# Performance work log

Measured on AMD Instinct MI355X. Metric: run time of the kernel, lower is better.

The kernel has to match this reference:

```python
import jax, jax.numpy as jnp
import numpy as np

USER_NUM = 100000
ITEM_NUM = 50000
N_EDGES = 2000000
EMB = 64
N_LAYERS = 3


def setup_inputs() -> dict:
    key = jax.random.key(0)
    k1, k2, k3, k4 = jax.random.split(key, 4)
    # xavier-uniform-like init scale for embeddings
    scale = float(np.sqrt(6.0 / (USER_NUM + EMB)))
    user_emb = jax.random.uniform(k1, (USER_NUM, EMB), jnp.float32, -scale, scale)
    scale_i = float(np.sqrt(6.0 / (ITEM_NUM + EMB)))
    item_emb = jax.random.uniform(k2, (ITEM_NUM, EMB), jnp.float32, -scale_i, scale_i)
    u_idx = jax.random.randint(k3, (N_EDGES,), 0, USER_NUM, jnp.int32)
    i_idx = jax.random.randint(k4, (N_EDGES,), 0, ITEM_NUM, jnp.int32)
    return {"user_emb": user_emb, "item_emb": item_emb, "u_idx": u_idx, "i_idx": i_idx}


def _degree_norms(u_idx, i_idx):
    ones = jnp.ones(u_idx.shape[0], jnp.float32)
    d_u = jax.ops.segment_sum(ones, u_idx, num_segments=USER_NUM)
    d_i = jax.ops.segment_sum(ones, i_idx, num_segments=ITEM_NUM)
    d_u = jnp.where(d_u == 0, 1.0, d_u)
    d_i = jnp.where(d_i == 0, 1.0, d_i)
    return ((1.0 / d_u)[:, None], (1.0 / d_i)[:, None],
            (d_u ** -0.5)[:, None], (d_i ** -0.5)[:, None])


def reference(user_emb, item_emb, u_idx, i_idx):
    d_u_inv, d_i_inv, d_u_inv_sqrt, d_i_inv_sqrt = _degree_norms(u_idx, i_idx)

    # SpMM via gather + segment_sum on the edge list (binary interaction values)
    def spmm_rt(x_u):  # (rt @ x_u): [U,D] -> [I,D]
        return jax.ops.segment_sum(x_u[u_idx], i_idx, num_segments=ITEM_NUM)

    def spmm_r(x_i):  # (r @ x_i): [I,D] -> [U,D]
        return jax.ops.segment_sum(x_i[i_idx], u_idx, num_segments=USER_NUM)

    user_e = user_emb
    item_e = item_emb
    sum_u = user_e
    sum_i = item_e
    for _ in range(N_LAYERS):
        # user propagation: u -> hyperedge(items) -> u
        tmp_u = user_e * d_u_inv_sqrt
        tmp_i = spmm_rt(tmp_u) * d_i_inv
        user_e = spmm_r(tmp_i) * d_u_inv_sqrt
        sum_u = sum_u + user_e
        # item propagation: i -> hyperedge(users) -> i
        tmp_i2 = item_e * d_i_inv_sqrt
        tmp_u2 = spmm_r(tmp_i2) * d_u_inv
        item_e = spmm_rt(tmp_u2) * d_i_inv_sqrt
        sum_i = sum_i + item_e
    inv = 1.0 / (N_LAYERS + 1)
    return sum_u * inv, sum_i * inv
```

## Files before the change

kernel.cpp:

```cpp
#include <hip/hip_runtime.h>
#include <hip/hip_fp16.h>
#include <math.h>

#define U_NUM 100000
#define I_NUM 50000
#define NE    2000000
#define EMB   64
#define NLAYERS 3

#define BSH   7
#define BROWS 128
#define NBU_U ((U_NUM + BROWS - 1) >> BSH)
#define NBU_I ((I_NUM + BROWS - 1) >> BSH)
#define NBU_T (NBU_U + NBU_I)
#define PACK_SH 17
#define PACK_MASK 0x1FFFF

#define CAP_U 4096
#define CAP_I 6144

#define CHUNK2 2048
#define NBLK2 ((NE + CHUNK2 - 1) / CHUNK2)

#define DBINS 512

#define ND_U ((U_NUM + 2047) / 2048)
#define ND_I ((I_NUM + 2047) / 2048)
#define NINIT (((U_NUM + I_NUM) * (EMB / 4) + 255) / 256)

#define FP8_SCALE 512.0f

typedef float v2f __attribute__((ext_vector_type(2)));

static inline int ceil_div(int a, int b){ return (a + b - 1) / b; }


__global__ void binfill_k(const int* __restrict__ u_idx, const int* __restrict__ i_idx,
                          int* __restrict__ bcur_u, int* __restrict__ bcur_i,
                          int* __restrict__ bin_u, int* __restrict__ bin_i){
  __shared__ int scnt[NBU_T];
  __shared__ int gbase[NBU_T];
  __shared__ int scur[NBU_T];
  int t = threadIdx.x;
  for (int k = t; k < NBU_T; k += 256){ scnt[k] = 0; scur[k] = 0; }
  __syncthreads();
  int e0 = blockIdx.x * CHUNK2 + t * 8;
  int u[8], iv[8];
  bool act = e0 < NE;
  if (act){
    int4 a = *(const int4*)(u_idx + e0);
    int4 b = *(const int4*)(u_idx + e0 + 4);
    int4 c = *(const int4*)(i_idx + e0);
    int4 d = *(const int4*)(i_idx + e0 + 4);
    u[0]=a.x; u[1]=a.y; u[2]=a.z; u[3]=a.w; u[4]=b.x; u[5]=b.y; u[6]=b.z; u[7]=b.w;
    iv[0]=c.x; iv[1]=c.y; iv[2]=c.z; iv[3]=c.w; iv[4]=d.x; iv[5]=d.y; iv[6]=d.z; iv[7]=d.w;
#pragma unroll
    for (int k = 0; k < 8; ++k){
      atomicAdd(&scnt[u[k] >> BSH], 1);
      atomicAdd(&scnt[NBU_U + (iv[k] >> BSH)], 1);
    }
  }
  __syncthreads();
  for (int k = t; k < NBU_T; k += 256){
    int c = scnt[k];
    if (c){
      int* bc = (k < NBU_U) ? (bcur_u + k) : (bcur_i + (k - NBU_U));
      gbase[k] = atomicAdd(bc, c);
    }
  }
  __syncthreads();
  if (act){
#pragma unroll
    for (int k = 0; k < 8; ++k){
      int bu = u[k] >> BSH;
      int p = atomicAdd(&scur[bu], 1);
      bin_u[(size_t)bu * CAP_U + gbase[bu] + p] =
          ((u[k] & (BROWS - 1)) << PACK_SH) | iv[k];
      int bi = NBU_U + (iv[k] >> BSH);
      int p2 = atomicAdd(&scur[bi], 1);
      bin_i[(size_t)(bi - NBU_U) * CAP_I + gbase[bi] + p2] =
          ((iv[k] & (BROWS - 1)) << PACK_SH) | u[k];
    }
  }
}

__global__ void small_scan2_k(const int* __restrict__ cA, int* __restrict__ oA,
                              int* __restrict__ rA, int nA,
                              const int* __restrict__ cB, int* __restrict__ oB,
                              int* __restrict__ rB, int nB){
  const int* cnt; int* offs; int* cur; int n;
  if (blockIdx.x == 0){ cnt = cA; offs = oA; cur = rA; n = nA; }
  else { cnt = cB; offs = oB; cur = rB; n = nB; }
  __shared__ int s[1024];
  int t = threadIdx.x;
  int v = (t < n) ? cnt[t] : 0;
  s[t] = v; __syncthreads();
  for (int o = 1; o < 1024; o <<= 1){
    int x = (t >= o) ? s[t - o] : 0;
    __syncthreads();
    s[t] += x;
    __syncthreads();
  }
  int excl = (t > 0) ? s[t - 1] : 0;
  if (t < n){ offs[t] = excl; cur[t] = excl; }
  if (t == n - 1) offs[n] = s[t];
}


__global__ void bucket_build_k(const int* __restrict__ bin_u, const int* __restrict__ bin_i,
                               const int* __restrict__ bcnt_u, const int* __restrict__ bcnt_i,
                               const int* __restrict__ boffs_u, const int* __restrict__ boffs_i,
                               int* __restrict__ cnt_u, int* __restrict__ cnt_i,
                               int* __restrict__ offs_u, int* __restrict__ offs_i,
                               float* __restrict__ du_inv, float* __restrict__ du_invs,
                               float* __restrict__ di_inv, float* __restrict__ di_invs,
                               int* __restrict__ adj_u, int* __restrict__ adj_i,
                               int* __restrict__ dhist_u, int* __restrict__ dhist_i){
  __shared__ int h[BROWS];
  __shared__ int part[256];
  __shared__ int dh[DBINS];
  int b = blockIdx.x;
  const int* bin; const int* bcnt; const int* boffs; int* cnt; int* offs;
  float* inv; float* invs; int* adj; int* dhist; int jj, nrows; size_t cap;
  if (b < NBU_U){
    bin = bin_u; bcnt = bcnt_u; boffs = boffs_u; cnt = cnt_u; offs = offs_u;
    inv = du_inv; invs = du_invs; adj = adj_u; dhist = dhist_u; jj = b; nrows = U_NUM; cap = CAP_U;
  } else {
    bin = bin_i; bcnt = bcnt_i; boffs = boffs_i; cnt = cnt_i; offs = offs_i;
    inv = di_inv; invs = di_invs; adj = adj_i; dhist = dhist_i; jj = b - NBU_U; nrows = I_NUM; cap = CAP_I;
  }
  int tid = threadIdx.x;
  int r0 = jj << BSH;
  const int* binb = bin + (size_t)jj * cap;
  int ne = bcnt[jj];
  int badj = boffs[jj];
  if (tid < BROWS) h[tid] = 0;
  for (int t = tid; t < DBINS; t += 256) dh[t] = 0;
  __syncthreads();
  for (int e = tid; e < ne; e += 256)
    atomicAdd(&h[((unsigned)binb[e]) >> PACK_SH], 1);
  __syncthreads();
  int c = (tid < BROWS) ? h[tid] : 0;
  part[tid] = c; __syncthreads();
  for (int o = 1; o < 256; o <<= 1){
    int x = (tid >= o) ? part[tid - o] : 0;
    __syncthreads();
    part[tid] += x;
    __syncthreads();
  }
  int excl = (tid > 0) ? part[tid - 1] : 0;
  if (tid < BROWS){
    h[tid] = excl;
    int row = r0 + tid;
    if (row < nrows){
      cnt[row] = c;
      offs[row] = badj + excl;
      float d = (c > 0) ? (float)c : 1.0f;
      inv[row]  = 1.0f / d;
      invs[row] = 1.0f / sqrtf(d);
      atomicAdd(&dh[min(c, DBINS - 1)], 1);
    } else if (row == nrows){
      offs[row] = badj + excl;
    }
  }
  __syncthreads();
  for (int e = tid; e < ne; e += 256){
    int v = binb[e];
    int slot = badj + atomicAdd(&h[((unsigned)v) >> PACK_SH], 1);
    adj[slot] = v & PACK_MASK;
  }
  __syncthreads();
  for (int t = tid; t < DBINS; t += 256) if (dh[t]) atomicAdd(&dhist[t], dh[t]);
}


__device__ __forceinline__ unsigned pack4_fp8(float a, float b, float c, float d){
  int p = 0;
  p = __builtin_amdgcn_cvt_pk_fp8_f32(a, b, p, false);
  p = __builtin_amdgcn_cvt_pk_fp8_f32(c, d, p, true);
  return (unsigned)p;
}

__device__ __forceinline__ void accq(float* a, uint2 q){
  v2f f0 = __builtin_amdgcn_cvt_pk_f32_fp8(q.x, false);
  v2f f1 = __builtin_amdgcn_cvt_pk_f32_fp8(q.x, true);
  v2f f2 = __builtin_amdgcn_cvt_pk_f32_fp8(q.y, false);
  v2f f3 = __builtin_amdgcn_cvt_pk_f32_fp8(q.y, true);
  a[0] += f0.x; a[1] += f0.y; a[2] += f1.x; a[3] += f1.y;
  a[4] += f2.x; a[5] += f2.y; a[6] += f3.x; a[7] += f3.y;
}


__global__ void post_k(const int* __restrict__ cnt_u, const int* __restrict__ offs_u,
                       const int* __restrict__ dhist_u, int* __restrict__ dcur_u,
                       int4* __restrict__ rd_u,
                       const int* __restrict__ cnt_i, const int* __restrict__ offs_i,
                       const int* __restrict__ dhist_i, int* __restrict__ dcur_i,
                       int4* __restrict__ rd_i,
                       const float* __restrict__ ue, const float* __restrict__ ie,
                       const float* __restrict__ dus, const float* __restrict__ dis,
                       float* __restrict__ out, unsigned char* __restrict__ u0,
                       unsigned char* __restrict__ i0){
  int b = blockIdx.x;
  int t = threadIdx.x;
  if (b >= ND_U + ND_I){
    int idx4 = (b - ND_U - ND_I) * 256 + t;
    const int nu4 = U_NUM * (EMB / 4);
    const int tot4 = (U_NUM + I_NUM) * (EMB / 4);
    if (idx4 >= tot4) return;
    const float* e; unsigned char* hp; float s; int loc;
    if (idx4 < nu4){ e = ue; hp = u0; loc = idx4; s = dus[idx4 >> 4] * FP8_SCALE; }
    else { e = ie; hp = i0; loc = idx4 - nu4; s = dis[(idx4 - nu4) >> 4] * FP8_SCALE; }
    float4 v = ((const float4*)e)[loc];
    ((float4*)out)[idx4] = make_float4(v.x * 0.25f, v.y * 0.25f, v.z * 0.25f, v.w * 0.25f);
    ((unsigned*)hp)[loc] = pack4_fp8(v.x * s, v.y * s, v.z * s, v.w * s);
    return;
  }
  const int* cnt; const int* offs; const int* dhist; int* dcur; int4* rd; int n, base;
  if (b < ND_U){ cnt = cnt_u; offs = offs_u; dhist = dhist_u; dcur = dcur_u; rd = rd_u; n = U_NUM; base = b * 2048; }
  else { cnt = cnt_i; offs = offs_i; dhist = dhist_i; dcur = dcur_i; rd = rd_i; n = I_NUM; base = (b - ND_U) * 2048; }
  __shared__ int sc[DBINS];
  __shared__ int h[DBINS];
  __shared__ int base_s[DBINS];
  sc[t] = dhist[t]; sc[t + 256] = dhist[t + 256];
  h[t] = 0; h[t + 256] = 0;
  __syncthreads();
  for (int o = 1; o < DBINS; o <<= 1){
    int x0 = (t >= o) ? sc[t - o] : 0;
    int x1 = ((t + 256) >= o) ? sc[t + 256 - o] : 0;
    __syncthreads();
    sc[t] += x0; sc[t + 256] += x1;
    __syncthreads();
  }
  int end = min(base + 2048, n);
  for (int r = base + t; r < end; r += 256)
    atomicAdd(&h[min(cnt[r], DBINS - 1)], 1);
  __syncthreads();
  for (int tt = t; tt < DBINS; tt += 256){
    int c = h[tt];
    int excl = tt ? sc[tt - 1] : 0;
    base_s[tt] = c ? (excl + atomicAdd(&dcur[tt], c)) : 0;
    h[tt] = 0;
  }
  __syncthreads();
  for (int r = base + t; r < end; r += 256){
    int c = cnt[r];
    int bb = min(c, DBINS - 1);
    int pos = base_s[bb] + atomicAdd(&h[bb], 1);
    int bg = offs[r];
    rd[n - 1 - pos] = make_int4(bg, bg + c, r, 0);
  }
}


__global__ void spmm_pair(
    const int4* __restrict__ rdA, const int* __restrict__ adjA,
    const unsigned char* __restrict__ srcA, const float* __restrict__ phA,
    unsigned char* __restrict__ dstA, int nA,
    const int4* __restrict__ rdB, const int* __restrict__ adjB,
    const unsigned char* __restrict__ srcB, const float* __restrict__ phB,
    unsigned char* __restrict__ dstB, int nB){
  int t = blockIdx.x * blockDim.x + threadIdx.x;
  int rid = t >> 3;
  int lane = t & 7;
  const int4* rd; const int* adj; const unsigned char* src; const float* ph;
  unsigned char* dst;
  if (rid < nA){
    rd = rdA; adj = adjA; src = srcA; ph = phA; dst = dstA;
  } else {
    rid -= nA;
    if (rid >= nB) return;
    rd = rdB; adj = adjB; src = srcB; ph = phB; dst = dstB;
  }
  int4 d = rd[rid];
  int beg = d.x, end = d.y, row = d.z;
  const unsigned char* sp8 = src + (size_t)(lane << 3);
  float acc[8];
#pragma unroll
  for (int k = 0; k < 8; ++k) acc[k] = 0.f;
  int j = beg;
  for (; j + 7 < end; j += 8){
    int n0 = adj[j],   n1 = adj[j+1], n2 = adj[j+2], n3 = adj[j+3];
    int n4 = adj[j+4], n5 = adj[j+5], n6 = adj[j+6], n7 = adj[j+7];
    uint2 q0 = *(const uint2*)(sp8 + (((size_t)n0) << 6));
    uint2 q1 = *(const uint2*)(sp8 + (((size_t)n1) << 6));
    uint2 q2 = *(const uint2*)(sp8 + (((size_t)n2) << 6));
    uint2 q3 = *(const uint2*)(sp8 + (((size_t)n3) << 6));
    uint2 q4 = *(const uint2*)(sp8 + (((size_t)n4) << 6));
    uint2 q5 = *(const uint2*)(sp8 + (((size_t)n5) << 6));
    uint2 q6 = *(const uint2*)(sp8 + (((size_t)n6) << 6));
    uint2 q7 = *(const uint2*)(sp8 + (((size_t)n7) << 6));
    accq(acc, q0); accq(acc, q1); accq(acc, q2); accq(acc, q3);
    accq(acc, q4); accq(acc, q5); accq(acc, q6); accq(acc, q7);
  }
  for (; j < end; ++j){
    int n0 = adj[j];
    uint2 q0 = *(const uint2*)(sp8 + (((size_t)n0) << 6));
    accq(acc, q0);
  }
  float phv = ph[row];
  unsigned lo = pack4_fp8(acc[0] * phv, acc[1] * phv, acc[2] * phv, acc[3] * phv);
  unsigned hi = pack4_fp8(acc[4] * phv, acc[5] * phv, acc[6] * phv, acc[7] * phv);
  *(uint2*)(dst + (((size_t)row) << 6) + (size_t)(lane << 3)) = make_uint2(lo, hi);
}


__global__ void merge_k(const unsigned char* __restrict__ u1, const unsigned char* __restrict__ u2,
                        const unsigned char* __restrict__ u3,
                        const unsigned char* __restrict__ i1, const unsigned char* __restrict__ i2,
                        const unsigned char* __restrict__ i3,
                        const float* __restrict__ du_inv, const float* __restrict__ du_invs,
                        const float* __restrict__ di_inv, const float* __restrict__ di_invs,
                        float* __restrict__ out){
  int idx4 = blockIdx.x * blockDim.x + threadIdx.x;
  const int nu4 = U_NUM * (EMB / 4);
  const int tot4 = (U_NUM + I_NUM) * (EMB / 4);
  if (idx4 >= tot4) return;
  const unsigned char *t1, *t2, *t3; float ratio; int loc;
  if (idx4 < nu4){
    t1 = u1; t2 = u2; t3 = u3; loc = idx4;
    int row = idx4 >> 4;
    ratio = (0.25f / FP8_SCALE) * du_invs[row] / du_inv[row];
  } else {
    loc = idx4 - nu4;
    t1 = i1; t2 = i2; t3 = i3;
    int row = loc >> 4;
    ratio = (0.25f / FP8_SCALE) * di_invs[row] / di_inv[row];
  }
  unsigned q1 = ((const unsigned*)t1)[loc];
  unsigned q2 = ((const unsigned*)t2)[loc];
  unsigned q3 = ((const unsigned*)t3)[loc];
  float4 o = ((float4*)out)[idx4];
  v2f a, b;
  a = __builtin_amdgcn_cvt_pk_f32_fp8(q1, false); b = __builtin_amdgcn_cvt_pk_f32_fp8(q1, true);
  o.x += ratio * a.x; o.y += ratio * a.y; o.z += ratio * b.x; o.w += ratio * b.y;
  a = __builtin_amdgcn_cvt_pk_f32_fp8(q2, false); b = __builtin_amdgcn_cvt_pk_f32_fp8(q2, true);
  o.x += ratio * a.x; o.y += ratio * a.y; o.z += ratio * b.x; o.w += ratio * b.y;
  a = __builtin_amdgcn_cvt_pk_f32_fp8(q3, false); b = __builtin_amdgcn_cvt_pk_f32_fp8(q3, true);
  o.x += ratio * a.x; o.y += ratio * a.y; o.z += ratio * b.x; o.w += ratio * b.y;
  ((float4*)out)[idx4] = o;
}


extern "C" void kernel_launch(void* const* d_in, const int* in_sizes, int n_in,
                              void* d_out, int out_size, void* d_ws, size_t ws_size,
                              hipStream_t stream){
  const float* user_emb = (const float*)d_in[0];
  const float* item_emb = (const float*)d_in[1];
  const int*   u_idx    = (const int*)d_in[2];
  const int*   i_idx    = (const int*)d_in[3];
  float* out = (float*)d_out;

  char* w = (char*)d_ws;
  size_t off = 0;
  auto alloc = [&](size_t bytes) -> void* {
    void* p = (void*)(w + off);
    off += (bytes + 255) & ~(size_t)255;
    return p;
  };
  int* zb      = (int*)alloc((size_t)(NBU_T + 4 * DBINS) * 4);
  int* bcur_u  = zb;
  int* bcur_i  = bcur_u + NBU_U;
  int* dhist_u = bcur_i + NBU_I;
  int* dhist_i = dhist_u + DBINS;
  int* dcur_u  = dhist_i + DBINS;
  int* dcur_i  = dcur_u + DBINS;
  int* boffs_u = (int*)alloc((size_t)(NBU_U + 1) * 4);
  int* boffs_i = (int*)alloc((size_t)(NBU_I + 1) * 4);
  int* scr_u   = (int*)alloc((size_t)NBU_U * 4);
  int* scr_i   = (int*)alloc((size_t)NBU_I * 4);
  int* cnt_u   = (int*)alloc((size_t)U_NUM * 4);
  int* cnt_i   = (int*)alloc((size_t)I_NUM * 4);
  int* offs_u  = (int*)alloc((size_t)(U_NUM + 1) * 4);
  int* offs_i  = (int*)alloc((size_t)(I_NUM + 1) * 4);
  int4* rd_u   = (int4*)alloc((size_t)U_NUM * 16);
  int4* rd_i   = (int4*)alloc((size_t)I_NUM * 16);
  int* adj_u   = (int*)alloc((size_t)NE * 4);
  int* adj_i   = (int*)alloc((size_t)NE * 4);
  float* du_inv  = (float*)alloc((size_t)U_NUM * 4);
  float* du_invs = (float*)alloc((size_t)U_NUM * 4);
  float* di_inv  = (float*)alloc((size_t)I_NUM * 4);
  float* di_invs = (float*)alloc((size_t)I_NUM * 4);
  const size_t URB = (size_t)U_NUM * EMB;
  const size_t IRB = (size_t)I_NUM * EMB;
  unsigned char* hreg = (unsigned char*)alloc(4 * URB + 4 * IRB + URB + IRB);
  unsigned char* u0 = hreg;
  unsigned char* u1 = u0 + URB;
  unsigned char* u2 = u1 + URB;
  unsigned char* u3 = u2 + URB;
  unsigned char* i0 = u3 + URB;
  unsigned char* i1 = i0 + IRB;
  unsigned char* i2 = i1 + IRB;
  unsigned char* i3 = i2 + IRB;
  unsigned char* tmp_i = i3 + IRB;
  unsigned char* tmp_u = tmp_i + IRB;
  int* bin_u = (int*)hreg;
  int* bin_i = bin_u + (size_t)NBU_U * CAP_U;

  hipMemsetAsync(zb, 0, (size_t)(NBU_T + 4 * DBINS) * 4, stream);
  binfill_k<<<NBLK2, 256, 0, stream>>>(u_idx, i_idx, bcur_u, bcur_i, bin_u, bin_i);
  small_scan2_k<<<2, 1024, 0, stream>>>(bcur_u, boffs_u, scr_u, NBU_U,
                                        bcur_i, boffs_i, scr_i, NBU_I);
  bucket_build_k<<<NBU_T, 256, 0, stream>>>(bin_u, bin_i, bcur_u, bcur_i,
                                            boffs_u, boffs_i,
                                            cnt_u, cnt_i, offs_u, offs_i,
                                            du_inv, du_invs, di_inv, di_invs,
                                            adj_u, adj_i, dhist_u, dhist_i);

  post_k<<<ND_U + ND_I + NINIT, 256, 0, stream>>>(
      cnt_u, offs_u, dhist_u, dcur_u, rd_u,
      cnt_i, offs_i, dhist_i, dcur_i, rd_i,
      user_emb, item_emb, du_invs, di_invs, out, u0, i0);

  const int pair_grid = ceil_div((U_NUM + I_NUM) * 8, 256);
  unsigned char* uls[4] = { u0, u1, u2, u3 };
  unsigned char* ils[4] = { i0, i1, i2, i3 };
  for (int l = 0; l < NLAYERS; ++l){
    spmm_pair<<<pair_grid, 256, 0, stream>>>(
        rd_i, adj_i, uls[l], di_inv, tmp_i, I_NUM,
        rd_u, adj_u, ils[l], du_inv, tmp_u, U_NUM);
    spmm_pair<<<pair_grid, 256, 0, stream>>>(
        rd_u, adj_u, tmp_i, du_inv, uls[l + 1], U_NUM,
        rd_i, adj_i, tmp_u, di_inv, ils[l + 1], I_NUM);
  }

  merge_k<<<NINIT, 256, 0, stream>>>(u1, u2, u3, i1, i2, i3,
                                     du_inv, du_invs, di_inv, di_invs, out);
}
```

Measured before the change: 492.1 us.

## Enlarge binfill and bucket_build blocks; defer layer-0 output to merge

binfill now processes 8192 edges per 1024-thread block, cutting block count and the per-block global atomics on bucket cursors. bucket_build uses 512 threads per block. The layer-0 contribution (emb*0.25) is no longer written to the output in post_k and read back in merge_k; merge_k reads the original fp32 embeddings directly. This removes one full-size output write and read, at the cost of more LDS and scan work per block and possibly lower occupancy.

Measured after the change: 468.8 us, median of 2. 4.7% less time.

```diff
diff --git a/kernel.cpp b/kernel.cpp
--- a/kernel.cpp
+++ b/kernel.cpp
@@ -19,10 +19,11 @@
 #define CAP_U 4096
 #define CAP_I 6144
 
-#define CHUNK2 2048
+#define CHUNK2 8192
 #define NBLK2 ((NE + CHUNK2 - 1) / CHUNK2)
 
 #define DBINS 512
+#define BBT   512
 
 #define ND_U ((U_NUM + 2047) / 2048)
 #define ND_I ((I_NUM + 2047) / 2048)
@@ -42,11 +43,13 @@
   __shared__ int gbase[NBU_T];
   __shared__ int scur[NBU_T];
   int t = threadIdx.x;
-  for (int k = t; k < NBU_T; k += 256){ scnt[k] = 0; scur[k] = 0; }
-  __syncthreads();
-  int e0 = blockIdx.x * CHUNK2 + t * 8;
+  for (int k = t; k < NBU_T; k += 1024){ scnt[k] = 0; scur[k] = 0; }
+  __syncthreads();
+  int base = blockIdx.x * CHUNK2;
+  int end = min(base + CHUNK2, NE);
+  int e0 = base + t * 8;
+  bool act = e0 < end;
   int u[8], iv[8];
-  bool act = e0 < NE;
   if (act){
     int4 a = *(const int4*)(u_idx + e0);
     int4 b = *(const int4*)(u_idx + e0 + 4);
@@ -61,7 +64,7 @@
     }
   }
   __syncthreads();
-  for (int k = t; k < NBU_T; k += 256){
+  for (int k = t; k < NBU_T; k += 1024){
     int c = scnt[k];
     if (c){
       int* bc = (k < NBU_U) ? (bcur_u + k) : (bcur_i + (k - NBU_U));
@@ -117,7 +120,7 @@
                                int* __restrict__ adj_u, int* __restrict__ adj_i,
                                int* __restrict__ dhist_u, int* __restrict__ dhist_i){
   __shared__ int h[BROWS];
-  __shared__ int part[256];
+  __shared__ int part[BBT];
   __shared__ int dh[DBINS];
   int b = blockIdx.x;
   const int* bin; const int* bcnt; const int* boffs; int* cnt; int* offs;
@@ -135,14 +138,14 @@
   int ne = bcnt[jj];
   int badj = boffs[jj];
   if (tid < BROWS) h[tid] = 0;
-  for (int t = tid; t < DBINS; t += 256) dh[t] = 0;
-  __syncthreads();
-  for (int e = tid; e < ne; e += 256)
+  if (tid < DBINS) dh[tid] = 0;
+  __syncthreads();
+  for (int e = tid; e < ne; e += BBT)
     atomicAdd(&h[((unsigned)binb[e]) >> PACK_SH], 1);
   __syncthreads();
   int c = (tid < BROWS) ? h[tid] : 0;
   part[tid] = c; __syncthreads();
-  for (int o = 1; o < 256; o <<= 1){
+  for (int o = 1; o < BBT; o <<= 1){
     int x = (tid >= o) ? part[tid - o] : 0;
     __syncthreads();
     part[tid] += x;
@@ -164,13 +167,13 @@
     }
   }
   __syncthreads();
-  for (int e = tid; e < ne; e += 256){
+  for (int e = tid; e < ne; e += BBT){
     int v = binb[e];
     int slot = badj + atomicAdd(&h[((unsigned)v) >> PACK_SH], 1);
     adj[slot] = v & PACK_MASK;
   }
   __syncthreads();
-  for (int t = tid; t < DBINS; t += 256) if (dh[t]) atomicAdd(&dhist[t], dh[t]);
+  if (tid < DBINS && dh[tid]) atomicAdd(&dhist[tid], dh[tid]);
 }
 
 
@@ -199,8 +202,7 @@
                        int4* __restrict__ rd_i,
                        const float* __restrict__ ue, const float* __restrict__ ie,
                        const float* __restrict__ dus, const float* __restrict__ dis,
-                       float* __restrict__ out, unsigned char* __restrict__ u0,
-                       unsigned char* __restrict__ i0){
+                       unsigned char* __restrict__ u0, unsigned char* __restrict__ i0){
   int b = blockIdx.x;
   int t = threadIdx.x;
   if (b >= ND_U + ND_I){
@@ -212,7 +214,6 @@
     if (idx4 < nu4){ e = ue; hp = u0; loc = idx4; s = dus[idx4 >> 4] * FP8_SCALE; }
     else { e = ie; hp = i0; loc = idx4 - nu4; s = dis[(idx4 - nu4) >> 4] * FP8_SCALE; }
     float4 v = ((const float4*)e)[loc];
-    ((float4*)out)[idx4] = make_float4(v.x * 0.25f, v.y * 0.25f, v.z * 0.25f, v.w * 0.25f);
     ((unsigned*)hp)[loc] = pack4_fp8(v.x * s, v.y * s, v.z * s, v.w * s);
     return;
   }
@@ -305,7 +306,8 @@
 }
 
 
-__global__ void merge_k(const unsigned char* __restrict__ u1, const unsigned char* __restrict__ u2,
+__global__ void merge_k(const float* __restrict__ ue, const float* __restrict__ ie,
+                        const unsigned char* __restrict__ u1, const unsigned char* __restrict__ u2,
                         const unsigned char* __restrict__ u3,
                         const unsigned char* __restrict__ i1, const unsigned char* __restrict__ i2,
                         const unsigned char* __restrict__ i3,
@@ -316,21 +318,22 @@
   const int nu4 = U_NUM * (EMB / 4);
   const int tot4 = (U_NUM + I_NUM) * (EMB / 4);
   if (idx4 >= tot4) return;
-  const unsigned char *t1, *t2, *t3; float ratio; int loc;
+  const float* e; const unsigned char *t1, *t2, *t3; float ratio; int loc;
   if (idx4 < nu4){
-    t1 = u1; t2 = u2; t3 = u3; loc = idx4;
+    e = ue; t1 = u1; t2 = u2; t3 = u3; loc = idx4;
     int row = idx4 >> 4;
     ratio = (0.25f / FP8_SCALE) * du_invs[row] / du_inv[row];
   } else {
     loc = idx4 - nu4;
-    t1 = i1; t2 = i2; t3 = i3;
+    e = ie; t1 = i1; t2 = i2; t3 = i3;
     int row = loc >> 4;
     ratio = (0.25f / FP8_SCALE) * di_invs[row] / di_inv[row];
   }
   unsigned q1 = ((const unsigned*)t1)[loc];
   unsigned q2 = ((const unsigned*)t2)[loc];
   unsigned q3 = ((const unsigned*)t3)[loc];
-  float4 o = ((float4*)out)[idx4];
+  float4 v = ((const float4*)e)[loc];
+  float4 o = make_float4(v.x * 0.25f, v.y * 0.25f, v.z * 0.25f, v.w * 0.25f);
   v2f a, b;
   a = __builtin_amdgcn_cvt_pk_f32_fp8(q1, false); b = __builtin_amdgcn_cvt_pk_f32_fp8(q1, true);
   o.x += ratio * a.x; o.y += ratio * a.y; o.z += ratio * b.x; o.w += ratio * b.y;
@@ -398,10 +401,10 @@
   int* bin_i = bin_u + (size_t)NBU_U * CAP_U;
 
   hipMemsetAsync(zb, 0, (size_t)(NBU_T + 4 * DBINS) * 4, stream);
-  binfill_k<<<NBLK2, 256, 0, stream>>>(u_idx, i_idx, bcur_u, bcur_i, bin_u, bin_i);
+  binfill_k<<<NBLK2, 1024, 0, stream>>>(u_idx, i_idx, bcur_u, bcur_i, bin_u, bin_i);
   small_scan2_k<<<2, 1024, 0, stream>>>(bcur_u, boffs_u, scr_u, NBU_U,
                                         bcur_i, boffs_i, scr_i, NBU_I);
-  bucket_build_k<<<NBU_T, 256, 0, stream>>>(bin_u, bin_i, bcur_u, bcur_i,
+  bucket_build_k<<<NBU_T, BBT, 0, stream>>>(bin_u, bin_i, bcur_u, bcur_i,
                                             boffs_u, boffs_i,
                                             cnt_u, cnt_i, offs_u, offs_i,
                                             du_inv, du_invs, di_inv, di_invs,
@@ -410,7 +413,7 @@
   post_k<<<ND_U + ND_I + NINIT, 256, 0, stream>>>(
       cnt_u, offs_u, dhist_u, dcur_u, rd_u,
       cnt_i, offs_i, dhist_i, dcur_i, rd_i,
-      user_emb, item_emb, du_invs, di_invs, out, u0, i0);
+      user_emb, item_emb, du_invs, di_invs, u0, i0);
 
   const int pair_grid = ceil_div((U_NUM + I_NUM) * 8, 256);
   unsigned char* uls[4] = { u0, u1, u2, u3 };
@@ -424,6 +427,6 @@
         rd_i, adj_i, tmp_u, di_inv, ils[l + 1], I_NUM);
   }
 
-  merge_k<<<NINIT, 256, 0, stream>>>(u1, u2, u3, i1, i2, i3,
+  merge_k<<<NINIT, 256, 0, stream>>>(user_emb, item_emb, u1, u2, u3, i1, i2, i3,
                                      du_inv, du_invs, di_inv, di_invs, out);
 }
```
